# Performance work log

Measured on AMD Instinct MI355X. Metric: run time of the kernel, lower is better.

## Reference

```python
import jax, jax.numpy as jnp
import numpy as np

B, T, C, H, D = 128, 256, 384, 6, 64  # batch, seq (block_size), embed_dim, heads, head_size
FF = 4 * C


def _layernorm(x, g, b, eps=1e-5):
    mu = jnp.mean(x, axis=-1, keepdims=True)
    var = jnp.var(x, axis=-1, keepdims=True)
    return (x - mu) * jax.lax.rsqrt(var + eps) * g + b


def setup_inputs() -> dict:
    key = jax.random.key(0)
    ks = jax.random.split(key, 16)
    w = lambda k, shape: (jax.random.normal(k, shape, jnp.float32) * 0.02)
    return {
        "x": jax.random.normal(ks[0], (B, T, C), jnp.float32),
        "ln1_g": jnp.ones((C,), jnp.float32),
        "ln1_b": jnp.zeros((C,), jnp.float32),
        "Wk": w(ks[1], (H, C, D)), "bk": jnp.zeros((H, D), jnp.float32),
        "Wq": w(ks[2], (H, C, D)), "bq": jnp.zeros((H, D), jnp.float32),
        "Wv": w(ks[3], (H, C, D)), "bv": jnp.zeros((H, D), jnp.float32),
        "Wp": w(ks[4], (C, C)), "bp": jnp.zeros((C,), jnp.float32),
        "ln2_g": jnp.ones((C,), jnp.float32),
        "ln2_b": jnp.zeros((C,), jnp.float32),
        "W1": w(ks[5], (C, FF)), "b1": jnp.zeros((FF,), jnp.float32),
        "W2": w(ks[6], (FF, C)), "b2": jnp.zeros((C,), jnp.float32),
    }


def reference(x, ln1_g, ln1_b, Wk, bk, Wq, bq, Wv, bv, Wp, bp, ln2_g, ln2_b, W1, b1, W2, b2):
    # pre-LN attention branch
    h = _layernorm(x, ln1_g, ln1_b)
    # per-head projections, batched over heads: (B,T,C) x (H,C,D) -> (B,H,T,D)
    K = jnp.einsum("btc,hcd->bhtd", h, Wk) + bk[None, :, None, :]
    Q = jnp.einsum("btc,hcd->bhtd", h, Wq) + bq[None, :, None, :]
    V = jnp.einsum("btc,hcd->bhtd", h, Wv) + bv[None, :, None, :]
    # NOTE: original computes K @ Q^T scaled by embed_dim**-0.5 (faithful quirk)
    scores = jnp.einsum("bhtd,bhsd->bhts", K, Q) * (C ** -0.5)
    causal = jnp.tril(jnp.ones((T, T), dtype=bool))  # keep s <= t
    scores = jnp.where(causal[None, None], scores, -jnp.inf)
    attn = jax.nn.softmax(scores, axis=-1)  # dropout = identity (eval mode)
    out = jnp.einsum("bhts,bhsd->bhtd", attn, V)
    out = out.transpose(0, 2, 1, 3).reshape(B, T, C)  # concat heads
    x = x + out @ Wp + bp
    # pre-LN FFN branch
    h2 = _layernorm(x, ln2_g, ln2_b)
    x = x + jax.nn.relu(h2 @ W1 + b1) @ W2 + b2
    return x
```

## Files before the change

### kernel.cpp

```cpp
#include <hip/hip_runtime.h>
#include <stdint.h>

#define BB 128
#define TT 256
#define CC 384
#define HH 6
#define DD 64
#define FFF 1536
#define ROWS (BB*TT)

#define FCH 16384
#define NFC (ROWS/FCH)

typedef unsigned short u16;
typedef __bf16 bf8v __attribute__((ext_vector_type(8)));
typedef float f4v __attribute__((ext_vector_type(4)));

__device__ __forceinline__ float bf2f(u16 u) {
    unsigned int v = ((unsigned int)u) << 16;
    float f;
    __builtin_memcpy(&f, &v, 4);
    return f;
}
__device__ __forceinline__ u16 f2bf(float f) {
    unsigned int u;
    __builtin_memcpy(&u, &f, 4);
    u += 0x7fffu + ((u >> 16) & 1u);
    return (u16)(u >> 16);
}

__device__ __forceinline__ void gload_lds16(const void* g, void* l) {
    __builtin_amdgcn_global_load_lds(
        (__attribute__((address_space(1))) void*)(g),
        (__attribute__((address_space(3))) void*)(l), 16, 0, 0);
}

__global__ __launch_bounds__(256) void ln_kernel(
    const float* __restrict__ x, const float* __restrict__ g,
    const float* __restrict__ b, u16* __restrict__ out)
{
    const int row  = blockIdx.x * 4 + (threadIdx.x >> 6);
    const int lane = threadIdx.x & 63;
    const float* xr = x + (long long)row * CC;
    float v[6]; float s = 0.f;
#pragma unroll
    for (int i = 0; i < 6; ++i) { v[i] = xr[lane + i * 64]; s += v[i]; }
#pragma unroll
    for (int o = 32; o > 0; o >>= 1) s += __shfl_xor(s, o);
    const float mu = s * (1.f / CC);
    float q = 0.f;
#pragma unroll
    for (int i = 0; i < 6; ++i) { float d = v[i] - mu; q += d * d; }
#pragma unroll
    for (int o = 32; o > 0; o >>= 1) q += __shfl_xor(q, o);
    const float inv = rsqrtf(q * (1.f / CC) + 1e-5f);
    u16* orow = out + (long long)row * CC;
#pragma unroll
    for (int i = 0; i < 6; ++i) {
        int c = lane + i * 64;
        orow[c] = f2bf((v[i] - mu) * inv * g[c] + b[c]);
    }
}

__global__ __launch_bounds__(256) void cvt_weights(
    const float* __restrict__ Wq, const float* __restrict__ Wk, const float* __restrict__ Wv,
    const float* __restrict__ bq, const float* __restrict__ bk, const float* __restrict__ bv,
    const float* __restrict__ Wp, const float* __restrict__ W1, const float* __restrict__ W2,
    u16* __restrict__ wqkvT, u16* __restrict__ wpT, u16* __restrict__ w1T,
    u16* __restrict__ w2T, float* __restrict__ bqkv)
{
    const int S0 = 1152 * 384, S1 = 384 * 384, S2 = 1536 * 384, S3 = 384 * 1536;
    int i = blockIdx.x * 256 + threadIdx.x;
    if (i < S0) {
        int n = i / 384, k = i % 384;
        const float* W = (n < 384) ? Wq : (n < 768) ? Wk : Wv;
        int nn = (n >= 768) ? n - 768 : (n >= 384) ? n - 384 : n;
        int h = nn >> 6, d = nn & 63;
        wqkvT[i] = f2bf(W[h * (384 * 64) + k * 64 + d]);
        return;
    }
    i -= S0;
    if (i < S1) { int n = i / 384, k = i % 384; wpT[i] = f2bf(Wp[k * 384 + n]); return; }
    i -= S1;
    if (i < S2) { int n = i / 384, k = i % 384; w1T[i] = f2bf(W1[k * 1536 + n]); return; }
    i -= S2;
    if (i < S3) { int n = i / 1536, k = i % 1536; w2T[i] = f2bf(W2[k * 384 + n]); return; }
    i -= S3;
    if (i < 1152) bqkv[i] = (i < 384) ? bq[i] : (i < 768) ? bk[i - 384] : bv[i - 768];
}

__global__ __launch_bounds__(256) void vtrans_kernel(
    const u16* __restrict__ qkv, u16* __restrict__ vt)
{
    __shared__ u16 tile[64][65];
    const int z = blockIdx.x;
    const int tb = blockIdx.y;
    const int zb = z / HH, zh = z % HH;
    const u16* src = qkv + ((long long)(zb * TT + tb * 64)) * 1152 + 768 + zh * 64;
    const int tid = threadIdx.x;
#pragma unroll
    for (int it = 0; it < 16; ++it) {
        int idx = it * 256 + tid; int tl = idx >> 6, d = idx & 63;
        tile[tl][d] = src[(long long)tl * 1152 + d];
    }
    __syncthreads();
    u16* dst = vt + (long long)z * 64 * 256 + tb * 64;
#pragma unroll
    for (int it = 0; it < 16; ++it) {
        int idx = it * 256 + tid; int d = idx >> 6, tl = idx & 63;
        dst[(long long)d * 256 + tl] = tile[tl][d];
    }
}

__global__ __launch_bounds__(256) void flash_kernel(
    const u16* __restrict__ qkv, const u16* __restrict__ vt, u16* __restrict__ attnout)
{
    __shared__ __align__(16) u16 Pl[128 * 72];

    const int bh = blockIdx.x;
    const int half = blockIdx.y;
    const int b = bh / HH, hh = bh % HH;
    const int tid = threadIdx.x;
    const int wave = tid >> 6, lane = tid & 63;
    const int quad = lane >> 4, lq = lane & 15;
    const int t0 = half * 128;

    const long long qrow = (long long)b * TT * 1152;
    const u16* Kb  = qkv + qrow + 384 + hh * 64;
    const u16* Qb  = qkv + qrow + hh * 64;
    const u16* Vtb = vt + (long long)bh * (DD * TT);

    bf8v af[2][2];
#pragma unroll
    for (int i = 0; i < 2; ++i)
#pragma unroll
        for (int ks = 0; ks < 2; ++ks)
            af[i][ks] = *(const bf8v*)(Kb + (long long)(t0 + wave * 32 + i * 16 + lq) * 1152
                                          + ks * 32 + quad * 8);

    float m_run[2][4], l_run[2][4];
    f4v oacc[2][4];
#pragma unroll
    for (int i = 0; i < 2; ++i) {
#pragma unroll
        for (int r = 0; r < 4; ++r) { m_run[i][r] = -1e30f; l_run[i][r] = 0.f; }
#pragma unroll
        for (int j = 0; j < 4; ++j) oacc[i][j] = (f4v){0.f, 0.f, 0.f, 0.f};
    }

    const float scs = 0.05103103630798287f;
    const int ntiles = 2 * (half + 1);
    for (int st = 0; st < ntiles; ++st) {
        const int s0 = st * 64;
        f4v sacc[2][4];
#pragma unroll
        for (int i = 0; i < 2; ++i)
#pragma unroll
            for (int j = 0; j < 4; ++j) sacc[i][j] = (f4v){0.f, 0.f, 0.f, 0.f};
#pragma unroll
        for (int ks = 0; ks < 2; ++ks) {
            bf8v bq[4];
#pragma unroll
            for (int j = 0; j < 4; ++j)
                bq[j] = *(const bf8v*)(Qb + (long long)(s0 + j * 16 + lq) * 1152
                                          + ks * 32 + quad * 8);
#pragma unroll
            for (int i = 0; i < 2; ++i)
#pragma unroll
                for (int j = 0; j < 4; ++j)
                    sacc[i][j] = __builtin_amdgcn_mfma_f32_16x16x32_bf16(af[i][ks], bq[j], sacc[i][j], 0, 0, 0);
        }
#pragma unroll
        for (int i = 0; i < 2; ++i)
#pragma unroll
            for (int j = 0; j < 4; ++j)
#pragma unroll
                for (int r = 0; r < 4; ++r) {
                    int t_g = t0 + wave * 32 + i * 16 + quad * 4 + r;
                    int s_g = s0 + j * 16 + lq;
                    float v = sacc[i][j][r] * scs;
                    sacc[i][j][r] = (s_g <= t_g) ? v : -1e30f;
                }
#pragma unroll
        for (int i = 0; i < 2; ++i)
#pragma unroll
            for (int r = 0; r < 4; ++r) {
                float mt = sacc[i][0][r];
#pragma unroll
                for (int j = 1; j < 4; ++j) mt = fmaxf(mt, sacc[i][j][r]);
#pragma unroll
                for (int o = 8; o > 0; o >>= 1) mt = fmaxf(mt, __shfl_xor(mt, o));
                const float mn = fmaxf(m_run[i][r], mt);
                const float alpha = __expf(m_run[i][r] - mn);
                float rs = 0.f;
#pragma unroll
                for (int j = 0; j < 4; ++j) {
                    float e = __expf(sacc[i][j][r] - mn);
                    sacc[i][j][r] = e; rs += e;
                }
#pragma unroll
                for (int o = 8; o > 0; o >>= 1) rs += __shfl_xor(rs, o);
                m_run[i][r] = mn;
                l_run[i][r] = l_run[i][r] * alpha + rs;
#pragma unroll
                for (int j = 0; j < 4; ++j) oacc[i][j][r] *= alpha;
            }
#pragma unroll
        for (int i = 0; i < 2; ++i)
#pragma unroll
            for (int j = 0; j < 4; ++j)
#pragma unroll
                for (int r = 0; r < 4; ++r)
                    Pl[(wave * 32 + i * 16 + quad * 4 + r) * 72 + j * 16 + lq] = f2bf(sacc[i][j][r]);
#pragma unroll
        for (int ks2 = 0; ks2 < 2; ++ks2) {
            bf8v ap[2], bv_[4];
#pragma unroll
            for (int i = 0; i < 2; ++i)
                ap[i] = *(const bf8v*)(Pl + (wave * 32 + i * 16 + lq) * 72 + ks2 * 32 + quad * 8);
#pragma unroll
            for (int j = 0; j < 4; ++j)
                bv_[j] = *(const bf8v*)(Vtb + (long long)(j * 16 + lq) * 256 + s0 + ks2 * 32 + quad * 8);
#pragma unroll
            for (int i = 0; i < 2; ++i)
#pragma unroll
                for (int j = 0; j < 4; ++j)
                    oacc[i][j] = __builtin_amdgcn_mfma_f32_16x16x32_bf16(ap[i], bv_[j], oacc[i][j], 0, 0, 0);
        }
    }
#pragma unroll
    for (int i = 0; i < 2; ++i)
#pragma unroll
        for (int r = 0; r < 4; ++r) {
            const float inv = 1.f / l_run[i][r];
            u16* orow = attnout + ((long long)(b * TT + t0 + wave * 32 + i * 16 + quad * 4 + r)) * CC + hh * 64;
#pragma unroll
            for (int j = 0; j < 4; ++j)
                orow[j * 16 + lq] = f2bf(oacc[i][j][r] * inv);
        }
}

template<int BM, int BN, bool OUTBF, bool RELU, bool HASRES>
__global__ __launch_bounds__(256) void gemm_bt(
    const u16* __restrict__ A, const u16* __restrict__ Bw, void* __restrict__ Cp,
    const float* __restrict__ bias, const float* __restrict__ res,
    int K, int lda, int ldb, int ldc,
    long long sAb, long long sAh, long long sBb, long long sBh,
    long long sCb, long long sCh, int Hb, float scale)
{
    __shared__ __align__(16) u16 As[BM * 32];
    __shared__ __align__(16) u16 Bs[BN * 32];

    const int tid = threadIdx.x;
    const int wave = tid >> 6, lane = tid & 63;
    const int quad = lane >> 4, lq = lane & 15;

    const int z = blockIdx.z;
    const int zb = z / Hb, zh = z % Hb;
    const int m0 = blockIdx.x * BM;
    const int n0 = blockIdx.y * BN;

    A  += (long long)zb * sAb + (long long)zh * sAh + (long long)m0 * lda;
    Bw += (long long)zb * sBb + (long long)zh * sBh + (long long)n0 * ldb;
    const long long coff = (long long)zb * sCb + (long long)zh * sCh;

    constexpr int WM = BM / 2, WN = BN / 2;
    constexpr int MT = WM / 16, NT = WN / 16;
    const int wm0 = (wave >> 1) * WM;
    const int wn0 = (wave & 1) * WN;

    f4v acc[MT][NT];
#pragma unroll
    for (int i = 0; i < MT; ++i)
#pragma unroll
        for (int j = 0; j < NT; ++j) acc[i][j] = (f4v){0.f, 0.f, 0.f, 0.f};

    constexpr int AIT = BM / 64;
    constexpr int BIT = BN / 64;

    for (int k0 = 0; k0 < K; k0 += 32) {
        __syncthreads();
#pragma unroll
        for (int j = 0; j < AIT; ++j) {
            int idx = j * 256 + tid; int r = idx >> 2, c = idx & 3;
            gload_lds16(A + (long long)r * lda + k0 + c * 8, As + idx * 8);
        }
#pragma unroll
        for (int j = 0; j < BIT; ++j) {
            int idx = j * 256 + tid; int r = idx >> 2, c = idx & 3;
            gload_lds16(Bw + (long long)r * ldb + k0 + c * 8, Bs + idx * 8);
        }
        __syncthreads();

        bf8v af[MT], bfr[NT];
#pragma unroll
        for (int i = 0; i < MT; ++i)
            af[i] = *(const bf8v*)(As + (wm0 + i * 16 + lq) * 32 + quad * 8);
#pragma unroll
        for (int j = 0; j < NT; ++j)
            bfr[j] = *(const bf8v*)(Bs + (wn0 + j * 16 + lq) * 32 + quad * 8);
#pragma unroll
        for (int i = 0; i < MT; ++i)
#pragma unroll
            for (int j = 0; j < NT; ++j)
                acc[i][j] = __builtin_amdgcn_mfma_f32_16x16x32_bf16(af[i], bfr[j], acc[i][j], 0, 0, 0);
    }

#pragma unroll
    for (int i = 0; i < MT; ++i) {
#pragma unroll
        for (int j = 0; j < NT; ++j) {
            const int gcol = n0 + wn0 + j * 16 + lq;
            const float bcol = bias ? bias[gcol] : 0.f;
#pragma unroll
            for (int r = 0; r < 4; ++r) {
                const int grow = m0 + wm0 + i * 16 + quad * 4 + r;
                const long long off = coff + (long long)grow * ldc + gcol;
                float v = acc[i][j][r] * scale + bcol;
                if (HASRES) v += res[off];
                if (RELU)   v = fmaxf(v, 0.f);
                if (OUTBF)  ((u16*)Cp)[off] = f2bf(v);
                else        ((float*)Cp)[off] = v;
            }
        }
    }
}

extern "C" void kernel_launch(void* const* d_in, const int* in_sizes, int n_in,
                              void* d_out, int out_size, void* d_ws, size_t ws_size,
                              hipStream_t stream)
{
    const float* x    = (const float*)d_in[0];
    const float* ln1g = (const float*)d_in[1];
    const float* ln1b = (const float*)d_in[2];
    const float* Wk   = (const float*)d_in[3];
    const float* bk   = (const float*)d_in[4];
    const float* Wq   = (const float*)d_in[5];
    const float* bq   = (const float*)d_in[6];
    const float* Wv   = (const float*)d_in[7];
    const float* bv   = (const float*)d_in[8];
    const float* Wp   = (const float*)d_in[9];
    const float* bp   = (const float*)d_in[10];
    const float* ln2g = (const float*)d_in[11];
    const float* ln2b = (const float*)d_in[12];
    const float* W1   = (const float*)d_in[13];
    const float* b1   = (const float*)d_in[14];
    const float* W2   = (const float*)d_in[15];
    const float* b2   = (const float*)d_in[16];

    char* ws = (char*)d_ws;
    size_t off = 0;
    auto alloc = [&](size_t bytes) -> char* {
        char* p = ws + off; off += (bytes + 255) & ~(size_t)255; return p;
    };
    u16*   wqkvT = (u16*)alloc((size_t)1152 * 384 * 2);
    u16*   wpT   = (u16*)alloc((size_t)384 * 384 * 2);
    u16*   w1T   = (u16*)alloc((size_t)1536 * 384 * 2);
    u16*   w2T   = (u16*)alloc((size_t)384 * 1536 * 2);
    float* bqkv  = (float*)alloc((size_t)1152 * 4);
    u16*   h     = (u16*)alloc((size_t)ROWS * CC * 2);
    u16*   qkv   = (u16*)alloc((size_t)ROWS * 1152 * 2);
    u16*   vtff  = (u16*)alloc((size_t)FCH * FFF * 2);
    u16* attnout = h;
    u16* h2      = h;
    float* x1    = (float*)qkv;
    u16*   vt    = vtff;
    u16*   ff    = vtff;

    ln_kernel<<<ROWS / 4, 256, 0, stream>>>(x, ln1g, ln1b, h);
    cvt_weights<<<6918, 256, 0, stream>>>(Wq, Wk, Wv, bq, bk, bv, Wp, W1, W2,
                                          wqkvT, wpT, w1T, w2T, bqkv);
    gemm_bt<128, 128, true, false, false><<<dim3(ROWS / 128, 1152 / 128, 1), 256, 0, stream>>>(
        h, wqkvT, qkv, bqkv, nullptr, 384, 384, 384, 1152,
        0, 0, 0, 0, 0, 0, 1, 1.f);
    vtrans_kernel<<<dim3(BB * HH, 4), 256, 0, stream>>>(qkv, vt);
    flash_kernel<<<dim3(BB * HH, 2), 256, 0, stream>>>(qkv, vt, attnout);
    gemm_bt<128, 128, false, false, true><<<dim3(ROWS / 128, CC / 128, 1), 256, 0, stream>>>(
        attnout, wpT, x1, bp, x, CC, CC, CC, CC,
        0, 0, 0, 0, 0, 0, 1, 1.f);
    ln_kernel<<<ROWS / 4, 256, 0, stream>>>(x1, ln2g, ln2b, h2);
    for (int fc = 0; fc < NFC; ++fc) {
        const long long ro = (long long)fc * FCH;
        gemm_bt<128, 128, true, true, false><<<dim3(FCH / 128, FFF / 128, 1), 256, 0, stream>>>(
            h2 + ro * CC, w1T, ff, b1, nullptr, CC, CC, CC, FFF,
            0, 0, 0, 0, 0, 0, 1, 1.f);
        gemm_bt<128, 128, false, false, true><<<dim3(FCH / 128, CC / 128, 1), 256, 0, stream>>>(
            ff, w2T, (float*)d_out + ro * CC, b2, x1 + ro * CC, FFF, FFF, FFF, CC,
            0, 0, 0, 0, 0, 0, 1, 1.f);
    }
}
```

Before: 449.6 us.

## Double GEMM K-tile to 64 and fuse LN1 with weight conversion kernel

Doubles the K-step of the shared bf16 GEMM from 32 to 64, so each pair of barriers covers two MFMA sub-steps. This halves the number of synchronisation rounds and load issues per output tile. It also merges the first layernorm and the weight-conversion kernel into one launch, dispatching on block index. The cost is doubled LDS per block (32 KB), which may reduce occupancy, and row stride 64 may raise LDS bank conflicts.

```diff
diff --git a/kernel.cpp b/kernel.cpp
--- a/kernel.cpp
+++ b/kernel.cpp
@@ -35,48 +35,59 @@
         (__attribute__((address_space(3))) void*)(l), 16, 0, 0);
 }
 
+__device__ __forceinline__ void ln_body(
+    int row, const float* __restrict__ x, const float* __restrict__ g,
+    const float* __restrict__ b, u16* __restrict__ out, int lane)
+{
+    const float* xr = x + (long long)row * CC;
+    float v[6]; float s = 0.f;
+#pragma unroll
+    for (int i = 0; i < 6; ++i) { v[i] = xr[lane + i * 64]; s += v[i]; }
+#pragma unroll
+    for (int o = 32; o > 0; o >>= 1) s += __shfl_xor(s, o);
+    const float mu = s * (1.f / CC);
+    float q = 0.f;
+#pragma unroll
+    for (int i = 0; i < 6; ++i) { float d = v[i] - mu; q += d * d; }
+#pragma unroll
+    for (int o = 32; o > 0; o >>= 1) q += __shfl_xor(q, o);
+    const float inv = rsqrtf(q * (1.f / CC) + 1e-5f);
+    u16* orow = out + (long long)row * CC;
+#pragma unroll
+    for (int i = 0; i < 6; ++i) {
+        int c = lane + i * 64;
+        orow[c] = f2bf((v[i] - mu) * inv * g[c] + b[c]);
+    }
+}
+
 __global__ __launch_bounds__(256) void ln_kernel(
     const float* __restrict__ x, const float* __restrict__ g,
     const float* __restrict__ b, u16* __restrict__ out)
 {
-    const int row  = blockIdx.x * 4 + (threadIdx.x >> 6);
-    const int lane = threadIdx.x & 63;
-    const float* xr = x + (long long)row * CC;
-    float v[6]; float s = 0.f;
-#pragma unroll
-    for (int i = 0; i < 6; ++i) { v[i] = xr[lane + i * 64]; s += v[i]; }
-#pragma unroll
-    for (int o = 32; o > 0; o >>= 1) s += __shfl_xor(s, o);
-    const float mu = s * (1.f / CC);
-    float q = 0.f;
-#pragma unroll
-    for (int i = 0; i < 6; ++i) { float d = v[i] - mu; q += d * d; }
-#pragma unroll
-    for (int o = 32; o > 0; o >>= 1) q += __shfl_xor(q, o);
-    const float inv = rsqrtf(q * (1.f / CC) + 1e-5f);
-    u16* orow = out + (long long)row * CC;
-#pragma unroll
-    for (int i = 0; i < 6; ++i) {
-        int c = lane + i * 64;
-        orow[c] = f2bf((v[i] - mu) * inv * g[c] + b[c]);
-    }
-}
-
-__global__ __launch_bounds__(256) void cvt_weights(
+    ln_body(blockIdx.x * 4 + (threadIdx.x >> 6), x, g, b, out, threadIdx.x & 63);
+}
+
+__global__ __launch_bounds__(256) void ln1_cvt_kernel(
+    const float* __restrict__ x, const float* __restrict__ ln1g, const float* __restrict__ ln1b,
+    u16* __restrict__ h,
     const float* __restrict__ Wq, const float* __restrict__ Wk, const float* __restrict__ Wv,
     const float* __restrict__ bq, const float* __restrict__ bk, const float* __restrict__ bv,
     const float* __restrict__ Wp, const float* __restrict__ W1, const float* __restrict__ W2,
     u16* __restrict__ wqkvT, u16* __restrict__ wpT, u16* __restrict__ w1T,
     u16* __restrict__ w2T, float* __restrict__ bqkv)
 {
+    if (blockIdx.x < ROWS / 4) {
+        ln_body(blockIdx.x * 4 + (threadIdx.x >> 6), x, ln1g, ln1b, h, threadIdx.x & 63);
+        return;
+    }
     const int S0 = 1152 * 384, S1 = 384 * 384, S2 = 1536 * 384, S3 = 384 * 1536;
-    int i = blockIdx.x * 256 + threadIdx.x;
+    int i = (blockIdx.x - ROWS / 4) * 256 + threadIdx.x;
     if (i < S0) {
         int n = i / 384, k = i % 384;
         const float* W = (n < 384) ? Wq : (n < 768) ? Wk : Wv;
         int nn = (n >= 768) ? n - 768 : (n >= 384) ? n - 384 : n;
-        int h = nn >> 6, d = nn & 63;
-        wqkvT[i] = f2bf(W[h * (384 * 64) + k * 64 + d]);
+        int hh = nn >> 6, d = nn & 63;
+        wqkvT[i] = f2bf(W[hh * (384 * 64) + k * 64 + d]);
         return;
     }
     i -= S0;
@@ -248,8 +259,8 @@
     long long sAb, long long sAh, long long sBb, long long sBh,
     long long sCb, long long sCh, int Hb, float scale)
 {
-    __shared__ __align__(16) u16 As[BM * 32];
-    __shared__ __align__(16) u16 Bs[BN * 32];
+    __shared__ __align__(16) u16 As[BM * 64];
+    __shared__ __align__(16) u16 Bs[BN * 64];
 
     const int tid = threadIdx.x;
     const int wave = tid >> 6, lane = tid & 63;
@@ -275,35 +286,38 @@
 #pragma unroll
         for (int j = 0; j < NT; ++j) acc[i][j] = (f4v){0.f, 0.f, 0.f, 0.f};
 
-    constexpr int AIT = BM / 64;
-    constexpr int BIT = BN / 64;
-
-    for (int k0 = 0; k0 < K; k0 += 32) {
+    constexpr int AIT = BM / 32;
+    constexpr int BIT = BN / 32;
+
+    for (int k0 = 0; k0 < K; k0 += 64) {
         __syncthreads();
 #pragma unroll
         for (int j = 0; j < AIT; ++j) {
-            int idx = j * 256 + tid; int r = idx >> 2, c = idx & 3;
+            int idx = j * 256 + tid; int r = idx >> 3, c = idx & 7;
             gload_lds16(A + (long long)r * lda + k0 + c * 8, As + idx * 8);
         }
 #pragma unroll
         for (int j = 0; j < BIT; ++j) {
-            int idx = j * 256 + tid; int r = idx >> 2, c = idx & 3;
+            int idx = j * 256 + tid; int r = idx >> 3, c = idx & 7;
             gload_lds16(Bw + (long long)r * ldb + k0 + c * 8, Bs + idx * 8);
         }
         __syncthreads();
 
-        bf8v af[MT], bfr[NT];
-#pragma unroll
-        for (int i = 0; i < MT; ++i)
-            af[i] = *(const bf8v*)(As + (wm0 + i * 16 + lq) * 32 + quad * 8);
-#pragma unroll
-        for (int j = 0; j < NT; ++j)
-            bfr[j] = *(const bf8v*)(Bs + (wn0 + j * 16 + lq) * 32 + quad * 8);
-#pragma unroll
-        for (int i = 0; i < MT; ++i)
+#pragma unroll
+        for (int ks = 0; ks < 2; ++ks) {
+            bf8v af[MT], bfr[NT];
+#pragma unroll
+            for (int i = 0; i < MT; ++i)
+                af[i] = *(const bf8v*)(As + (wm0 + i * 16 + lq) * 64 + ks * 32 + quad * 8);
 #pragma unroll
             for (int j = 0; j < NT; ++j)
-                acc[i][j] = __builtin_amdgcn_mfma_f32_16x16x32_bf16(af[i], bfr[j], acc[i][j], 0, 0, 0);
+                bfr[j] = *(const bf8v*)(Bs + (wn0 + j * 16 + lq) * 64 + ks * 32 + quad * 8);
+#pragma unroll
+            for (int i = 0; i < MT; ++i)
+#pragma unroll
+                for (int j = 0; j < NT; ++j)
+                    acc[i][j] = __builtin_amdgcn_mfma_f32_16x16x32_bf16(af[i], bfr[j], acc[i][j], 0, 0, 0);
+        }
     }
 
 #pragma unroll
@@ -367,9 +381,9 @@
     u16*   vt    = vtff;
     u16*   ff    = vtff;
 
-    ln_kernel<<<ROWS / 4, 256, 0, stream>>>(x, ln1g, ln1b, h);
-    cvt_weights<<<6918, 256, 0, stream>>>(Wq, Wk, Wv, bq, bk, bv, Wp, W1, W2,
-                                          wqkvT, wpT, w1T, w2T, bqkv);
+    ln1_cvt_kernel<<<ROWS / 4 + 6918, 256, 0, stream>>>(
+        x, ln1g, ln1b, h, Wq, Wk, Wv, bq, bk, bv, Wp, W1, W2,
+        wqkvT, wpT, w1T, w2T, bqkv);
     gemm_bt<128, 128, true, false, false><<<dim3(ROWS / 128, 1152 / 128, 1), 256, 0, stream>>>(
         h, wqkvT, qkv, bqkv, nullptr, 384, 384, 384, 1152,
         0, 0, 0, 0, 0, 0, 1, 1.f);
```

Result: slower. 470.7 us (+4.7%).
